# Optimization experiments

Measured on AMD Instinct MI355X. Metric: run time of the kernel, lower is better.

The kernel has to match this reference:

```python
import jax, jax.numpy as jnp
import numpy as np

EMBED_DIM = 1024
NUM_HEADS = 16
HEAD_DIM = EMBED_DIM // NUM_HEADS
B, T = 4, 2048


def setup_inputs() -> dict:
    key = jax.random.key(0)
    k1, k2, k3, k4, k5 = jax.random.split(key, 5)
    s = 0.02
    return {
        "x": jax.random.normal(k1, (B, T, EMBED_DIM), dtype=jnp.float32),
        "w_qkv": jax.random.normal(k2, (EMBED_DIM, 3 * EMBED_DIM), dtype=jnp.float32) * s,
        "b_qkv": jnp.zeros((3 * EMBED_DIM,), dtype=jnp.float32),
        "w_proj": jax.random.normal(k3, (EMBED_DIM, EMBED_DIM), dtype=jnp.float32) * s,
        "b_proj": jnp.zeros((EMBED_DIM,), dtype=jnp.float32),
    }


def reference(x, w_qkv, b_qkv, w_proj, b_proj):
    Bx, Tx, C = x.shape
    H, D = NUM_HEADS, HEAD_DIM
    qkv = x @ w_qkv + b_qkv                      # [B,T,3C]
    qkv = qkv.reshape(Bx, Tx, 3, H, D)
    q = qkv[:, :, 0].transpose(0, 2, 1, 3)       # [B,H,T,D]
    k = qkv[:, :, 1].transpose(0, 2, 1, 3)
    v = qkv[:, :, 2].transpose(0, 2, 1, 3)
    scale = 1.0 / jnp.sqrt(jnp.asarray(D, dtype=x.dtype))
    att = jnp.einsum("bhqd,bhkd->bhqk", q, k) * scale   # [B,H,T,T]
    causal = jnp.tril(jnp.ones((Tx, Tx), dtype=bool))
    att = jnp.where(causal[None, None], att, jnp.asarray(-jnp.inf, dtype=att.dtype))
    att = jax.nn.softmax(att, axis=-1)
    y = jnp.einsum("bhqk,bhkd->bhqd", att, v)            # [B,H,T,D]
    y = y.transpose(0, 2, 1, 3).reshape(Bx, Tx, C)
    return y @ w_proj + b_proj
```

## Files before the change

### kernel.cpp

```cpp
#include <hip/hip_runtime.h>
#include <hip/hip_bf16.h>

typedef __bf16 bf16_t;
typedef __attribute__((ext_vector_type(4))) __bf16 bf16x4;
typedef __attribute__((ext_vector_type(8))) __bf16 bf16x8;
typedef __attribute__((ext_vector_type(4))) float f32x4;
typedef __attribute__((ext_vector_type(16))) float f32x16;
typedef __attribute__((ext_vector_type(4))) unsigned int uint4v;

__device__ __forceinline__ void async_copy16(const void* g, void* lds) {
  __builtin_amdgcn_global_load_lds(
      (const __attribute__((address_space(1))) unsigned int*)g,
      (__attribute__((address_space(3))) unsigned int*)lds, 16, 0, 0);
}

__device__ __forceinline__ unsigned pkbf(float lo, float hi) {
  unsigned short a = __builtin_bit_cast(unsigned short, (bf16_t)lo);
  unsigned short b = __builtin_bit_cast(unsigned short, (bf16_t)hi);
  return (unsigned)a | ((unsigned)b << 16);
}

__device__ __forceinline__ float swap_max(float v) {
  return fmaxf(v, __shfl_xor(v, 32));
}
__device__ __forceinline__ float swap_add(float v) {
  return v + __shfl_xor(v, 32);
}

__global__ __launch_bounds__(256) void cast_f32_bf16(
    const float* __restrict__ in, bf16_t* __restrict__ out, long n8) {
  long i = (long)blockIdx.x * blockDim.x + threadIdx.x;
  if (i >= n8) return;
  const float4* p = (const float4*)(in + i * 8);
  float4 a = p[0], b = p[1];
  bf16x8 o;
  o[0] = (bf16_t)a.x; o[1] = (bf16_t)a.y; o[2] = (bf16_t)a.z; o[3] = (bf16_t)a.w;
  o[4] = (bf16_t)b.x; o[5] = (bf16_t)b.y; o[6] = (bf16_t)b.z; o[7] = (bf16_t)b.w;
  *(bf16x8*)(out + i * 8) = o;
}

__global__ __launch_bounds__(256) void transpose_cast(
    const float* __restrict__ in, bf16_t* __restrict__ out, int R, int C) {
  __shared__ float tile[32][33];
  int r0 = blockIdx.y * 32, c0 = blockIdx.x * 32;
  int tx = threadIdx.x, ty = threadIdx.y;
#pragma unroll
  for (int j = 0; j < 32; j += 8)
    tile[ty + j][tx] = in[(size_t)(r0 + ty + j) * C + c0 + tx];
  __syncthreads();
#pragma unroll
  for (int j = 0; j < 32; j += 8)
    out[(size_t)(c0 + ty + j) * R + r0 + tx] = (bf16_t)tile[tx][ty + j];
}

template <int MODE>
__global__ __launch_bounds__(256) void gemm_bf16(
    const bf16_t* __restrict__ A, const bf16_t* __restrict__ Bt,
    const float* __restrict__ bias, int M, int N, int K,
    bf16_t* __restrict__ Qo, bf16_t* __restrict__ Ko, bf16_t* __restrict__ Vo,
    float* __restrict__ Fo) {
  constexpr int BK = 64;
  __shared__ bf16_t As[128 * BK];
  __shared__ bf16_t Bs[128 * BK];
  const int tid = threadIdx.x;
  const int wid = tid >> 6, lane = tid & 63;
  const int wr = wid >> 1, wc = wid & 1;
  const int g = lane >> 4, c = lane & 15;
  const int m0 = blockIdx.y * 128, n0 = blockIdx.x * 128;
  const int lrow = lane >> 3;
  const int lseg = lane & 7;

  f32x4 acc[4][4] = {};

  for (int kt = 0; kt < K; kt += BK) {
#pragma unroll
    for (int cc = 0; cc < 4; ++cc) {
      int chunk = cc * 4 + wid;
      int row = chunk * 8 + lrow;
      int seg = lseg ^ (row & 7);
      async_copy16(A + (size_t)(m0 + row) * K + kt + seg * 8, &As[chunk * 512]);
    }
#pragma unroll
    for (int cc = 0; cc < 4; ++cc) {
      int chunk = cc * 4 + wid;
      int row = chunk * 8 + lrow;
      int seg = lseg ^ (row & 7);
      async_copy16(Bt + (size_t)(n0 + row) * K + kt + seg * 8, &Bs[chunk * 512]);
    }
    __syncthreads();
#pragma unroll
    for (int ks = 0; ks < 2; ++ks) {
      bf16x8 af[4], bfr[4];
#pragma unroll
      for (int m = 0; m < 4; ++m) {
        int row = wr * 64 + m * 16 + c;
        int seg = (ks * 4 + g) ^ (row & 7);
        af[m] = *(const bf16x8*)&As[row * 64 + seg * 8];
      }
#pragma unroll
      for (int n = 0; n < 4; ++n) {
        int row = wc * 64 + n * 16 + c;
        int seg = (ks * 4 + g) ^ (row & 7);
        bfr[n] = *(const bf16x8*)&Bs[row * 64 + seg * 8];
      }
#pragma unroll
      for (int m = 0; m < 4; ++m)
#pragma unroll
        for (int n = 0; n < 4; ++n)
          acc[m][n] =
              __builtin_amdgcn_mfma_f32_16x16x32_bf16(af[m], bfr[n], acc[m][n], 0, 0, 0);
    }
    __syncthreads();
  }

  if (MODE == 1) {
#pragma unroll
    for (int m = 0; m < 4; ++m) {
      int grow = m0 + wr * 64 + m * 16 + g * 4;
#pragma unroll
      for (int n = 0; n < 4; ++n) {
        int gcol = n0 + wc * 64 + n * 16 + c;
        float bs = bias[gcol];
#pragma unroll
        for (int i = 0; i < 4; ++i)
          Fo[(size_t)(grow + i) * N + gcol] = acc[m][n][i] + bs;
      }
    }
  } else {
#pragma unroll
    for (int m = 0; m < 4; ++m) {
      int grow = m0 + wr * 64 + m * 16 + g * 4;
#pragma unroll
      for (int n = 0; n < 4; ++n) {
        int gcol = n0 + wc * 64 + n * 16 + c;
        float bs = bias[gcol];
        int sel = gcol >> 10;
        int h = (gcol >> 6) & 15;
        int d = gcol & 63;
        if (sel < 2) {
          bf16_t* dst = (sel == 0) ? Qo : Ko;
#pragma unroll
          for (int i = 0; i < 4; ++i) {
            int row = grow + i;
            int b = row >> 11, t = row & 2047;
            dst[(((size_t)(b * 16 + h)) * 2048 + t) * 64 + d] = (bf16_t)(acc[m][n][i] + bs);
          }
        } else {
          int b = grow >> 11, t = grow & 2047;
          bf16x4 v;
#pragma unroll
          for (int i = 0; i < 4; ++i) v[i] = (bf16_t)(acc[m][n][i] + bs);
          *(bf16x4*)&Vo[(((size_t)(b * 16 + h)) * 64 + d) * 2048 + t] = v;
        }
      }
    }
  }
}

__global__ __launch_bounds__(256) void attn_fwd(
    const bf16_t* __restrict__ Qg_, const bf16_t* __restrict__ Kg_,
    const bf16_t* __restrict__ Vtg_, bf16_t* __restrict__ Y) {
  __shared__ bf16_t Ks[2][64 * 64];
  __shared__ bf16_t Vs[2][64 * 64];
  const int tid = threadIdx.x, wid = tid >> 6, lane = tid & 63;
  const int l31 = lane & 31, hi = lane >> 5;
  const int bh = blockIdx.x, pair = blockIdx.y;
  const int b = bh >> 4, h = bh & 15;
  const bf16_t* Qg = Qg_ + (size_t)bh * 2048 * 64;
  const bf16_t* Kg = Kg_ + (size_t)bh * 2048 * 64;
  const bf16_t* Vtg = Vtg_ + (size_t)bh * 64 * 2048;
  const float sc2 = 0.125f * 1.44269504088896f;

  for (int half = 0; half < 2; ++half) {
    const int qt = half ? (15 - pair) : pair;
    const int q0 = qt * 128;
    const int qw = q0 + wid * 32 + l31;
    const int qmaxw = q0 + wid * 32 + 31;
    const int NT = 2 * qt + 2;

    bf16x8 qf[4];
#pragma unroll
    for (int ks = 0; ks < 4; ++ks)
      qf[ks] = *(const bf16x8*)&Qg[(size_t)qw * 64 + ks * 16 + hi * 8];

    float m = -1e30f, l = 0.f;
    f32x16 ot0 = {}, ot1 = {};

#pragma unroll
    for (int cc = 0; cc < 2; ++cc) {
      int chunk = wid * 2 + cc;
      int row = chunk * 8 + (lane >> 3);
      int seg = (lane & 7) ^ (row & 7);
      async_copy16(Kg + (size_t)row * 64 + seg * 8, &Ks[0][chunk * 512]);
      async_copy16(Vtg + (size_t)row * 2048 + seg * 8, &Vs[0][chunk * 512]);
    }
    __syncthreads();

    for (int kt = 0; kt < NT; ++kt) {
      const int buf = kt & 1;
      if (kt + 1 < NT) {
#pragma unroll
        for (int cc = 0; cc < 2; ++cc) {
          int chunk = wid * 2 + cc;
          int row = chunk * 8 + (lane >> 3);
          int seg = (lane & 7) ^ (row & 7);
          async_copy16(Kg + (size_t)((kt + 1) * 64 + row) * 64 + seg * 8,
                       &Ks[buf ^ 1][chunk * 512]);
          async_copy16(Vtg + (size_t)row * 2048 + (kt + 1) * 64 + seg * 8,
                       &Vs[buf ^ 1][chunk * 512]);
        }
      }
      const int kv0 = kt * 64;
      if (kv0 <= qmaxw) {
        f32x16 st0 = {}, st1 = {};
#pragma unroll
        for (int ks = 0; ks < 4; ++ks) {
          int segb = ks * 2 + hi;
          {
            int row = l31;
            bf16x8 kf = *(const bf16x8*)&Ks[buf][row * 64 + (segb ^ (row & 7)) * 8];
            st0 = __builtin_amdgcn_mfma_f32_32x32x16_bf16(kf, qf[ks], st0, 0, 0, 0);
          }
          {
            int row = 32 + l31;
            bf16x8 kf = *(const bf16x8*)&Ks[buf][row * 64 + (segb ^ (row & 7)) * 8];
            st1 = __builtin_amdgcn_mfma_f32_32x32x16_bf16(kf, qf[ks], st1, 0, 0, 0);
          }
        }
        if (kv0 + 63 > qw) {
#pragma unroll
          for (int r = 0; r < 16; ++r) {
            int kvl = (r & 3) + 8 * (r >> 2) + 4 * hi;
            if (kv0 + kvl > qw) st0[r] = -1e30f;
            if (kv0 + 32 + kvl > qw) st1[r] = -1e30f;
          }
        }
        float pm = st0[0];
#pragma unroll
        for (int r = 1; r < 16; ++r) pm = fmaxf(pm, st0[r]);
#pragma unroll
        for (int r = 0; r < 16; ++r) pm = fmaxf(pm, st1[r]);
        pm = swap_max(pm);
        float mn = fmaxf(m, pm);
        float alpha = exp2f((m - mn) * sc2);
        m = mn;
        float rs = 0.f;
#pragma unroll
        for (int r = 0; r < 16; ++r) {
          st0[r] = exp2f((st0[r] - mn) * sc2);
          st1[r] = exp2f((st1[r] - mn) * sc2);
          rs += st0[r] + st1[r];
        }
        l = l * alpha + swap_add(rs);
#pragma unroll
        for (int r = 0; r < 16; ++r) { ot0[r] *= alpha; ot1[r] *= alpha; }
        bf16x8 pb[4];
#pragma unroll
        for (int nt = 0; nt < 2; ++nt) {
#pragma unroll
          for (int s = 0; s < 2; ++s) {
            float p0 = nt ? st1[8 * s + 0] : st0[8 * s + 0];
            float p1 = nt ? st1[8 * s + 1] : st0[8 * s + 1];
            float p2 = nt ? st1[8 * s + 2] : st0[8 * s + 2];
            float p3 = nt ? st1[8 * s + 3] : st0[8 * s + 3];
            float p4 = nt ? st1[8 * s + 4] : st0[8 * s + 4];
            float p5 = nt ? st1[8 * s + 5] : st0[8 * s + 5];
            float p6 = nt ? st1[8 * s + 6] : st0[8 * s + 6];
            float p7 = nt ? st1[8 * s + 7] : st0[8 * s + 7];
            unsigned a0 = pkbf(p0, p1), a1 = pkbf(p2, p3);
            unsigned b0 = pkbf(p4, p5), b1 = pkbf(p6, p7);
            unsigned t0 = (unsigned)__shfl_xor((int)(hi ? a0 : b0), 32);
            unsigned t1 = (unsigned)__shfl_xor((int)(hi ? a1 : b1), 32);
            uint4v words;
            words[0] = hi ? t0 : a0;
            words[1] = hi ? t1 : a1;
            words[2] = hi ? b0 : t0;
            words[3] = hi ? b1 : t1;
            pb[nt * 2 + s] = __builtin_bit_cast(bf16x8, words);
          }
        }
#pragma unroll
        for (int ks2 = 0; ks2 < 4; ++ks2) {
          int segb = ks2 * 2 + hi;
          {
            int row = l31;
            bf16x8 vf = *(const bf16x8*)&Vs[buf][row * 64 + (segb ^ (row & 7)) * 8];
            ot0 = __builtin_amdgcn_mfma_f32_32x32x16_bf16(vf, pb[ks2], ot0, 0, 0, 0);
          }
          {
            int row = 32 + l31;
            bf16x8 vf = *(const bf16x8*)&Vs[buf][row * 64 + (segb ^ (row & 7)) * 8];
            ot1 = __builtin_amdgcn_mfma_f32_32x32x16_bf16(vf, pb[ks2], ot1, 0, 0, 0);
          }
        }
      }
      __syncthreads();
    }

    float inv = 1.0f / l;
    size_t yrow = ((size_t)b * 2048 + qw) * 1024 + h * 64;
#pragma unroll
    for (int rq = 0; rq < 4; ++rq) {
      int dbase = 8 * rq + 4 * hi;
      bf16x4 v0, v1;
#pragma unroll
      for (int j = 0; j < 4; ++j) {
        v0[j] = (bf16_t)(ot0[rq * 4 + j] * inv);
        v1[j] = (bf16_t)(ot1[rq * 4 + j] * inv);
      }
      *(bf16x4*)&Y[yrow + dbase] = v0;
      *(bf16x4*)&Y[yrow + 32 + dbase] = v1;
    }
  }
}

extern "C" void kernel_launch(void* const* d_in, const int* in_sizes, int n_in,
                              void* d_out, int out_size, void* d_ws, size_t ws_size,
                              hipStream_t stream) {
  (void)in_sizes; (void)n_in; (void)out_size; (void)ws_size;
  const float* x = (const float*)d_in[0];
  const float* w_qkv = (const float*)d_in[1];
  const float* b_qkv = (const float*)d_in[2];
  const float* w_proj = (const float*)d_in[3];
  const float* b_proj = (const float*)d_in[4];
  float* out = (float*)d_out;

  char* ws = (char*)d_ws;
  size_t off = 0;
  bf16_t* xb = (bf16_t*)(ws + off); off += (size_t)8192 * 1024 * 2;
  bf16_t* wqkvT = (bf16_t*)(ws + off); off += (size_t)3072 * 1024 * 2;
  bf16_t* wprojT = (bf16_t*)(ws + off); off += (size_t)1024 * 1024 * 2;
  bf16_t* Qb = (bf16_t*)(ws + off); off += (size_t)8192 * 1024 * 2;
  bf16_t* Kb = (bf16_t*)(ws + off); off += (size_t)8192 * 1024 * 2;
  bf16_t* Vtb = (bf16_t*)(ws + off); off += (size_t)8192 * 1024 * 2;
  bf16_t* Yb = xb;

  cast_f32_bf16<<<4096, 256, 0, stream>>>(x, xb, (long)8192 * 1024 / 8);
  transpose_cast<<<dim3(96, 32), dim3(32, 8), 0, stream>>>(w_qkv, wqkvT, 1024, 3072);
  transpose_cast<<<dim3(32, 32), dim3(32, 8), 0, stream>>>(w_proj, wprojT, 1024, 1024);
  gemm_bf16<0><<<dim3(24, 64), 256, 0, stream>>>(xb, wqkvT, b_qkv, 8192, 3072, 1024,
                                                 Qb, Kb, Vtb, nullptr);
  attn_fwd<<<dim3(64, 8), 256, 0, stream>>>(Qb, Kb, Vtb, Yb);
  gemm_bf16<1><<<dim3(8, 64), 256, 0, stream>>>(Yb, wprojT, b_proj, 8192, 1024, 1024,
                                                nullptr, nullptr, nullptr, out);
}
```

Baseline: 206.3 us.

## Launch one attention block per query tile with lazy rescaling and MFMA priority

The attention kernel no longer pairs two causal query tiles per block. It launches 16 query-tile blocks per head, longest tiles first, and sets launch_bounds to 4 blocks per CU to raise occupancy. Online-softmax rescaling now runs only when the running max grows by more than a threshold, which skips most accumulator rescales. Max and sum reductions become trees, the exp step uses fma, and s_setprio raises priority around the MFMA sections. The trade-offs are more blocks with uneven work, a launch-bounds register cap that may cause spills, and the small numeric-range risk that lazy rescaling accepts.

```diff
diff --git a/kernel.cpp b/kernel.cpp
--- a/kernel.cpp
+++ b/kernel.cpp
@@ -157,160 +157,175 @@
   }
 }
 
-__global__ __launch_bounds__(256) void attn_fwd(
+__global__ __launch_bounds__(256, 4) void attn_fwd(
     const bf16_t* __restrict__ Qg_, const bf16_t* __restrict__ Kg_,
     const bf16_t* __restrict__ Vtg_, bf16_t* __restrict__ Y) {
   __shared__ bf16_t Ks[2][64 * 64];
   __shared__ bf16_t Vs[2][64 * 64];
   const int tid = threadIdx.x, wid = tid >> 6, lane = tid & 63;
   const int l31 = lane & 31, hi = lane >> 5;
-  const int bh = blockIdx.x, pair = blockIdx.y;
+  const int bh = blockIdx.x;
   const int b = bh >> 4, h = bh & 15;
   const bf16_t* Qg = Qg_ + (size_t)bh * 2048 * 64;
   const bf16_t* Kg = Kg_ + (size_t)bh * 2048 * 64;
   const bf16_t* Vtg = Vtg_ + (size_t)bh * 64 * 2048;
   const float sc2 = 0.125f * 1.44269504088896f;
-
-  for (int half = 0; half < 2; ++half) {
-    const int qt = half ? (15 - pair) : pair;
-    const int q0 = qt * 128;
-    const int qw = q0 + wid * 32 + l31;
-    const int qmaxw = q0 + wid * 32 + 31;
-    const int NT = 2 * qt + 2;
-
-    bf16x8 qf[4];
-#pragma unroll
-    for (int ks = 0; ks < 4; ++ks)
-      qf[ks] = *(const bf16x8*)&Qg[(size_t)qw * 64 + ks * 16 + hi * 8];
-
-    float m = -1e30f, l = 0.f;
-    f32x16 ot0 = {}, ot1 = {};
-
-#pragma unroll
-    for (int cc = 0; cc < 2; ++cc) {
-      int chunk = wid * 2 + cc;
-      int row = chunk * 8 + (lane >> 3);
-      int seg = (lane & 7) ^ (row & 7);
-      async_copy16(Kg + (size_t)row * 64 + seg * 8, &Ks[0][chunk * 512]);
-      async_copy16(Vtg + (size_t)row * 2048 + seg * 8, &Vs[0][chunk * 512]);
+  const float THR = 8.0f / sc2;
+
+  const int qt = 15 - blockIdx.y;
+  const int q0 = qt * 128;
+  const int qw = q0 + wid * 32 + l31;
+  const int qmaxw = q0 + wid * 32 + 31;
+  const int NT = 2 * qt + 2;
+
+  bf16x8 qf[4];
+#pragma unroll
+  for (int ks = 0; ks < 4; ++ks)
+    qf[ks] = *(const bf16x8*)&Qg[(size_t)qw * 64 + ks * 16 + hi * 8];
+
+  float m = -1e30f, l = 0.f;
+  f32x16 ot0 = {}, ot1 = {};
+
+#pragma unroll
+  for (int cc = 0; cc < 2; ++cc) {
+    int chunk = wid * 2 + cc;
+    int row = chunk * 8 + (lane >> 3);
+    int seg = (lane & 7) ^ (row & 7);
+    async_copy16(Kg + (size_t)row * 64 + seg * 8, &Ks[0][chunk * 512]);
+    async_copy16(Vtg + (size_t)row * 2048 + seg * 8, &Vs[0][chunk * 512]);
+  }
+  __syncthreads();
+
+  for (int kt = 0; kt < NT; ++kt) {
+    const int buf = kt & 1;
+    if (kt + 1 < NT) {
+#pragma unroll
+      for (int cc = 0; cc < 2; ++cc) {
+        int chunk = wid * 2 + cc;
+        int row = chunk * 8 + (lane >> 3);
+        int seg = (lane & 7) ^ (row & 7);
+        async_copy16(Kg + (size_t)((kt + 1) * 64 + row) * 64 + seg * 8,
+                     &Ks[buf ^ 1][chunk * 512]);
+        async_copy16(Vtg + (size_t)row * 2048 + (kt + 1) * 64 + seg * 8,
+                     &Vs[buf ^ 1][chunk * 512]);
+      }
+    }
+    const int kv0 = kt * 64;
+    if (kv0 <= qmaxw) {
+      f32x16 st0 = {}, st1 = {};
+      __builtin_amdgcn_s_setprio(1);
+#pragma unroll
+      for (int ks = 0; ks < 4; ++ks) {
+        int segb = ks * 2 + hi;
+        {
+          int row = l31;
+          bf16x8 kf = *(const bf16x8*)&Ks[buf][row * 64 + (segb ^ (row & 7)) * 8];
+          st0 = __builtin_amdgcn_mfma_f32_32x32x16_bf16(kf, qf[ks], st0, 0, 0, 0);
+        }
+        {
+          int row = 32 + l31;
+          bf16x8 kf = *(const bf16x8*)&Ks[buf][row * 64 + (segb ^ (row & 7)) * 8];
+          st1 = __builtin_amdgcn_mfma_f32_32x32x16_bf16(kf, qf[ks], st1, 0, 0, 0);
+        }
+      }
+      __builtin_amdgcn_s_setprio(0);
+      if (kv0 + 63 > qw) {
+#pragma unroll
+        for (int r = 0; r < 16; ++r) {
+          int kvl = (r & 3) + 8 * (r >> 2) + 4 * hi;
+          if (kv0 + kvl > qw) st0[r] = -1e30f;
+          if (kv0 + 32 + kvl > qw) st1[r] = -1e30f;
+        }
+      }
+      float t16[16];
+#pragma unroll
+      for (int r = 0; r < 16; ++r) t16[r] = fmaxf(st0[r], st1[r]);
+#pragma unroll
+      for (int r = 0; r < 8; ++r) t16[r] = fmaxf(t16[r], t16[r + 8]);
+#pragma unroll
+      for (int r = 0; r < 4; ++r) t16[r] = fmaxf(t16[r], t16[r + 4]);
+      float pm = fmaxf(fmaxf(t16[0], t16[1]), fmaxf(t16[2], t16[3]));
+      pm = swap_max(pm);
+      if (!__all(pm - m <= THR)) {
+        float mn = fmaxf(m, pm);
+        float al = exp2f((m - mn) * sc2);
+        m = mn;
+        l *= al;
+#pragma unroll
+        for (int r = 0; r < 16; ++r) { ot0[r] *= al; ot1[r] *= al; }
+      }
+      const float nmsc = -m * sc2;
+      float s16[16];
+#pragma unroll
+      for (int r = 0; r < 16; ++r) {
+        st0[r] = exp2f(fmaf(st0[r], sc2, nmsc));
+        st1[r] = exp2f(fmaf(st1[r], sc2, nmsc));
+        s16[r] = st0[r] + st1[r];
+      }
+#pragma unroll
+      for (int r = 0; r < 8; ++r) s16[r] += s16[r + 8];
+#pragma unroll
+      for (int r = 0; r < 4; ++r) s16[r] += s16[r + 4];
+      float rs = (s16[0] + s16[1]) + (s16[2] + s16[3]);
+      l += swap_add(rs);
+      bf16x8 pb[4];
+#pragma unroll
+      for (int nt = 0; nt < 2; ++nt) {
+#pragma unroll
+        for (int s = 0; s < 2; ++s) {
+          float p0 = nt ? st1[8 * s + 0] : st0[8 * s + 0];
+          float p1 = nt ? st1[8 * s + 1] : st0[8 * s + 1];
+          float p2 = nt ? st1[8 * s + 2] : st0[8 * s + 2];
+          float p3 = nt ? st1[8 * s + 3] : st0[8 * s + 3];
+          float p4 = nt ? st1[8 * s + 4] : st0[8 * s + 4];
+          float p5 = nt ? st1[8 * s + 5] : st0[8 * s + 5];
+          float p6 = nt ? st1[8 * s + 6] : st0[8 * s + 6];
+          float p7 = nt ? st1[8 * s + 7] : st0[8 * s + 7];
+          unsigned a0 = pkbf(p0, p1), a1 = pkbf(p2, p3);
+          unsigned b0 = pkbf(p4, p5), b1 = pkbf(p6, p7);
+          unsigned t0 = (unsigned)__shfl_xor((int)(hi ? a0 : b0), 32);
+          unsigned t1 = (unsigned)__shfl_xor((int)(hi ? a1 : b1), 32);
+          uint4v words;
+          words[0] = hi ? t0 : a0;
+          words[1] = hi ? t1 : a1;
+          words[2] = hi ? b0 : t0;
+          words[3] = hi ? b1 : t1;
+          pb[nt * 2 + s] = __builtin_bit_cast(bf16x8, words);
+        }
+      }
+      __builtin_amdgcn_s_setprio(1);
+#pragma unroll
+      for (int ks2 = 0; ks2 < 4; ++ks2) {
+        int segb = ks2 * 2 + hi;
+        {
+          int row = l31;
+          bf16x8 vf = *(const bf16x8*)&Vs[buf][row * 64 + (segb ^ (row & 7)) * 8];
+          ot0 = __builtin_amdgcn_mfma_f32_32x32x16_bf16(vf, pb[ks2], ot0, 0, 0, 0);
+        }
+        {
+          int row = 32 + l31;
+          bf16x8 vf = *(const bf16x8*)&Vs[buf][row * 64 + (segb ^ (row & 7)) * 8];
+          ot1 = __builtin_amdgcn_mfma_f32_32x32x16_bf16(vf, pb[ks2], ot1, 0, 0, 0);
+        }
+      }
+      __builtin_amdgcn_s_setprio(0);
     }
     __syncthreads();
-
-    for (int kt = 0; kt < NT; ++kt) {
-      const int buf = kt & 1;
-      if (kt + 1 < NT) {
-#pragma unroll
-        for (int cc = 0; cc < 2; ++cc) {
-          int chunk = wid * 2 + cc;
-          int row = chunk * 8 + (lane >> 3);
-          int seg = (lane & 7) ^ (row & 7);
-          async_copy16(Kg + (size_t)((kt + 1) * 64 + row) * 64 + seg * 8,
-                       &Ks[buf ^ 1][chunk * 512]);
-          async_copy16(Vtg + (size_t)row * 2048 + (kt + 1) * 64 + seg * 8,
-                       &Vs[buf ^ 1][chunk * 512]);
-        }
-      }
-      const int kv0 = kt * 64;
-      if (kv0 <= qmaxw) {
-        f32x16 st0 = {}, st1 = {};
-#pragma unroll
-        for (int ks = 0; ks < 4; ++ks) {
-          int segb = ks * 2 + hi;
-          {
-            int row = l31;
-            bf16x8 kf = *(const bf16x8*)&Ks[buf][row * 64 + (segb ^ (row & 7)) * 8];
-            st0 = __builtin_amdgcn_mfma_f32_32x32x16_bf16(kf, qf[ks], st0, 0, 0, 0);
-          }
-          {
-            int row = 32 + l31;
-            bf16x8 kf = *(const bf16x8*)&Ks[buf][row * 64 + (segb ^ (row & 7)) * 8];
-            st1 = __builtin_amdgcn_mfma_f32_32x32x16_bf16(kf, qf[ks], st1, 0, 0, 0);
-          }
-        }
-        if (kv0 + 63 > qw) {
-#pragma unroll
-          for (int r = 0; r < 16; ++r) {
-            int kvl = (r & 3) + 8 * (r >> 2) + 4 * hi;
-            if (kv0 + kvl > qw) st0[r] = -1e30f;
-            if (kv0 + 32 + kvl > qw) st1[r] = -1e30f;
-          }
-        }
-        float pm = st0[0];
-#pragma unroll
-        for (int r = 1; r < 16; ++r) pm = fmaxf(pm, st0[r]);
-#pragma unroll
-        for (int r = 0; r < 16; ++r) pm = fmaxf(pm, st1[r]);
-        pm = swap_max(pm);
-        float mn = fmaxf(m, pm);
-        float alpha = exp2f((m - mn) * sc2);
-        m = mn;
-        float rs = 0.f;
-#pragma unroll
-        for (int r = 0; r < 16; ++r) {
-          st0[r] = exp2f((st0[r] - mn) * sc2);
-          st1[r] = exp2f((st1[r] - mn) * sc2);
-          rs += st0[r] + st1[r];
-        }
-        l = l * alpha + swap_add(rs);
-#pragma unroll
-        for (int r = 0; r < 16; ++r) { ot0[r] *= alpha; ot1[r] *= alpha; }
-        bf16x8 pb[4];
-#pragma unroll
-        for (int nt = 0; nt < 2; ++nt) {
-#pragma unroll
-          for (int s = 0; s < 2; ++s) {
-            float p0 = nt ? st1[8 * s + 0] : st0[8 * s + 0];
-            float p1 = nt ? st1[8 * s + 1] : st0[8 * s + 1];
-            float p2 = nt ? st1[8 * s + 2] : st0[8 * s + 2];
-            float p3 = nt ? st1[8 * s + 3] : st0[8 * s + 3];
-            float p4 = nt ? st1[8 * s + 4] : st0[8 * s + 4];
-            float p5 = nt ? st1[8 * s + 5] : st0[8 * s + 5];
-            float p6 = nt ? st1[8 * s + 6] : st0[8 * s + 6];
-            float p7 = nt ? st1[8 * s + 7] : st0[8 * s + 7];
-            unsigned a0 = pkbf(p0, p1), a1 = pkbf(p2, p3);
-            unsigned b0 = pkbf(p4, p5), b1 = pkbf(p6, p7);
-            unsigned t0 = (unsigned)__shfl_xor((int)(hi ? a0 : b0), 32);
-            unsigned t1 = (unsigned)__shfl_xor((int)(hi ? a1 : b1), 32);
-            uint4v words;
-            words[0] = hi ? t0 : a0;
-            words[1] = hi ? t1 : a1;
-            words[2] = hi ? b0 : t0;
-            words[3] = hi ? b1 : t1;
-            pb[nt * 2 + s] = __builtin_bit_cast(bf16x8, words);
-          }
-        }
-#pragma unroll
-        for (int ks2 = 0; ks2 < 4; ++ks2) {
-          int segb = ks2 * 2 + hi;
-          {
-            int row = l31;
-            bf16x8 vf = *(const bf16x8*)&Vs[buf][row * 64 + (segb ^ (row & 7)) * 8];
-            ot0 = __builtin_amdgcn_mfma_f32_32x32x16_bf16(vf, pb[ks2], ot0, 0, 0, 0);
-          }
-          {
-            int row = 32 + l31;
-            bf16x8 vf = *(const bf16x8*)&Vs[buf][row * 64 + (segb ^ (row & 7)) * 8];
-            ot1 = __builtin_amdgcn_mfma_f32_32x32x16_bf16(vf, pb[ks2], ot1, 0, 0, 0);
-          }
-        }
-      }
-      __syncthreads();
-    }
-
-    float inv = 1.0f / l;
-    size_t yrow = ((size_t)b * 2048 + qw) * 1024 + h * 64;
-#pragma unroll
-    for (int rq = 0; rq < 4; ++rq) {
-      int dbase = 8 * rq + 4 * hi;
-      bf16x4 v0, v1;
-#pragma unroll
-      for (int j = 0; j < 4; ++j) {
-        v0[j] = (bf16_t)(ot0[rq * 4 + j] * inv);
-        v1[j] = (bf16_t)(ot1[rq * 4 + j] * inv);
-      }
-      *(bf16x4*)&Y[yrow + dbase] = v0;
-      *(bf16x4*)&Y[yrow + 32 + dbase] = v1;
-    }
+  }
+
+  float inv = 1.0f / l;
+  size_t yrow = ((size_t)b * 2048 + qw) * 1024 + h * 64;
+#pragma unroll
+  for (int rq = 0; rq < 4; ++rq) {
+    int dbase = 8 * rq + 4 * hi;
+    bf16x4 v0, v1;
+#pragma unroll
+    for (int j = 0; j < 4; ++j) {
+      v0[j] = (bf16_t)(ot0[rq * 4 + j] * inv);
+      v1[j] = (bf16_t)(ot1[rq * 4 + j] * inv);
+    }
+    *(bf16x4*)&Y[yrow + dbase] = v0;
+    *(bf16x4*)&Y[yrow + 32 + dbase] = v1;
   }
 }
 
@@ -340,7 +355,7 @@
   transpose_cast<<<dim3(32, 32), dim3(32, 8), 0, stream>>>(w_proj, wprojT, 1024, 1024);
   gemm_bf16<0><<<dim3(24, 64), 256, 0, stream>>>(xb, wqkvT, b_qkv, 8192, 3072, 1024,
                                                  Qb, Kb, Vtb, nullptr);
-  attn_fwd<<<dim3(64, 8), 256, 0, stream>>>(Qb, Kb, Vtb, Yb);
+  attn_fwd<<<dim3(64, 16), 256, 0, stream>>>(Qb, Kb, Vtb, Yb);
   gemm_bf16<1><<<dim3(8, 64), 256, 0, stream>>>(Yb, wprojT, b_proj, 8192, 1024, 1024,
                                                 nullptr, nullptr, nullptr, out);
 }
```

After: 188.0 us (median of 2 runs). 8.9% less time.
